# Performance work log

Measured on AMD Instinct MI355X. Metric: run time of the kernel, lower is better.

Reference implementation:

```python
import jax, jax.numpy as jnp
import numpy as np

E, C, K, S = 8, 128, 512, 512  # embedding_dim, channels, kernel_size, stride
NEG_SLOPE = 0.01  # torch F.leaky_relu default


def setup_inputs() -> dict:
    key = jax.random.key(0)
    ks = jax.random.split(key, 11)
    B, T = 4, 1_000_000
    sc = 0.05
    return {
        "x": jax.random.normal(ks[0], (B, T, E), jnp.float32),
        # ctx_conv: Conv1d(E, 2C, K, stride=S) -> weight (2C, E, K), bias (2C,)
        "ctx_conv_w": jax.random.normal(ks[1], (2 * C, E, K), jnp.float32) * sc,
        "ctx_conv_b": jax.random.normal(ks[2], (2 * C,), jnp.float32) * sc,
        # ctx_share: Conv1d(C, C, 1) -> (C, C) pointwise
        "ctx_share_w": jax.random.normal(ks[3], (C, C), jnp.float32) * sc,
        "ctx_share_b": jax.random.normal(ks[4], (C,), jnp.float32) * sc,
        "main_conv_w": jax.random.normal(ks[5], (2 * C, E, K), jnp.float32) * sc,
        "main_conv_b": jax.random.normal(ks[6], (2 * C,), jnp.float32) * sc,
        "main_share_w": jax.random.normal(ks[7], (C, C), jnp.float32) * sc,
        "main_share_b": jax.random.normal(ks[8], (C,), jnp.float32) * sc,
        # gct_proj: Linear(C, C) -> weight (C, C) (y = g @ W.T + b)
        "gct_proj_w": jax.random.normal(ks[9], (C, C), jnp.float32) * sc,
        "gct_proj_b": jax.random.normal(ks[10], (C,), jnp.float32) * sc,
    }


def _leaky(x):
    return jnp.where(x >= 0, x, NEG_SLOPE * x)


def _glu(x):  # GLU over channel dim 1
    a, b = jnp.split(x, 2, axis=1)
    return a * jax.nn.sigmoid(b)


def _conv(z, w, b):
    # z: (B, Cin, T), w: (Cout, Cin, K) -> (B, Cout, T_out), stride S, VALID
    y = jax.lax.conv_general_dilated(z, w, (S,), 'VALID',
                                     dimension_numbers=('NCH', 'OIH', 'NCH'))
    return y + b[None, :, None]


def _branch_act(z, wc, bc, ws, bs):
    # glu(conv(z)) -> leaky_relu(1x1 share conv)
    h = _glu(_conv(z, wc, bc))                                   # (B, C, T_out)
    h = _leaky(jnp.einsum('oc,bct->bot', ws, h) + bs[None, :, None])
    return h


def reference(x, ctx_conv_w, ctx_conv_b, ctx_share_w, ctx_share_b,
              main_conv_w, main_conv_b, main_share_w, main_share_b,
              gct_proj_w, gct_proj_b):
    z = jnp.transpose(x, (0, 2, 1))  # (B, E, T)
    # Context branch: global max over time of ctx activations (GCG context).
    g = _branch_act(z, ctx_conv_w, ctx_conv_b, ctx_share_w, ctx_share_b)
    gct = jnp.max(g, axis=-1)  # (B, C)
    # Main branch with global channel gating.
    h = _branch_act(z, main_conv_w, main_conv_b, main_share_w, main_share_b)  # (B, C, T_out)
    q = jnp.tanh(gct @ gct_proj_w.T + gct_proj_b)                # (B, C)
    gate = jax.nn.sigmoid(jnp.einsum('bct,bc->bt', h, q))        # (B, T_out)
    out = jnp.max(h * gate[:, None, :], axis=-1)                 # (B, C)
    return out
```

## Files before the change

### kernel.cpp

```cpp
#include <hip/hip_runtime.h>
#include <hip/hip_bf16.h>
#include <cmath>

#define B_    4
#define T_    1000000
#define E_    8
#define C_    128
#define NCH   512
#define KK    4096
#define TOUT  1953
#define TP    1956
#define TPAD  2048
#define NT2   31

typedef __attribute__((ext_vector_type(8))) short bf16x8;
typedef __attribute__((ext_vector_type(4))) float f32x4;

__device__ __forceinline__ float sigmoidf_(float v) { return 1.f / (1.f + __expf(-v)); }

__device__ __forceinline__ void gl2lds16(const void* g, void* l) {
  __builtin_amdgcn_global_load_lds((const __attribute__((address_space(1))) void*)g,
                                   (__attribute__((address_space(3))) void*)l, 16, 0, 0);
}

__global__ __launch_bounds__(256) void convert_x(const float* __restrict__ x,
                                                 __hip_bfloat16* __restrict__ xb) {
  size_t gid = (size_t)blockIdx.x * 256 + threadIdx.x;
  size_t idx8 = gid * 8;
  size_t b = idx8 >> 23;
  size_t rem = idx8 & ((1ull << 23) - 1);
  union { __hip_bfloat16 h[8]; uint4 u; } o;
  if (rem < (size_t)TOUT * KK) {
    const float* src = x + b * 8000000ull + rem;
    float4 f0 = *(const float4*)(src);
    float4 f1 = *(const float4*)(src + 4);
    o.h[0] = __float2bfloat16(f0.x); o.h[1] = __float2bfloat16(f0.y);
    o.h[2] = __float2bfloat16(f0.z); o.h[3] = __float2bfloat16(f0.w);
    o.h[4] = __float2bfloat16(f1.x); o.h[5] = __float2bfloat16(f1.y);
    o.h[6] = __float2bfloat16(f1.z); o.h[7] = __float2bfloat16(f1.w);
  } else {
    o.u = make_uint4(0, 0, 0, 0);
  }
  *(uint4*)(xb + idx8) = o.u;
}

__global__ __launch_bounds__(256) void prep_w(
    const float* __restrict__ wc, const float* __restrict__ bc,
    const float* __restrict__ wm, const float* __restrict__ bm,
    __hip_bfloat16* __restrict__ Wtb, float* __restrict__ bias_t) {
  __shared__ float row[KK];
  int n = blockIdx.x;
  int br = n >> 8, o = n & 255;
  const float* wsrc = (br ? wm : wc) + (size_t)o * KK;
  for (int i = threadIdx.x; i < KK; i += 256) row[i] = wsrc[i];
  __syncthreads();
  for (int i = threadIdx.x; i < KK; i += 256) {
    int kpos = i >> 3, e = i & 7;
    Wtb[(size_t)n * KK + i] = __float2bfloat16(row[e * 512 + kpos]);
  }
  if (threadIdx.x == 0) bias_t[n] = (br ? bm : bc)[o];
}

__global__ __launch_bounds__(256) void mfma_gemm(
    const __hip_bfloat16* __restrict__ xb, const __hip_bfloat16* __restrict__ Wtb,
    const float* __restrict__ bias_t, float* __restrict__ u2) {
  __shared__ __hip_bfloat16 As[128 * 32];
  __shared__ __hip_bfloat16 Bs[128 * 32];
  const int tid  = threadIdx.x;
  const int lane = tid & 63, wave = tid >> 6;
  const int wm = wave >> 1, wn = wave & 1;
  const int n0 = blockIdx.x * 128;
  const int t0 = blockIdx.y * 128;
  const int b  = blockIdx.z;

  const int r0 = tid >> 2;
  const int q8 = (tid & 3) * 8;
  const __hip_bfloat16* aS = xb + ((size_t)b * TPAD + (t0 + r0)) * KK + q8;
  const __hip_bfloat16* bS = Wtb + (size_t)(n0 + r0) * KK + q8;
  __hip_bfloat16* aD0 = As + (wave * 64) * 8;
  __hip_bfloat16* aD1 = As + (256 + wave * 64) * 8;
  __hip_bfloat16* bD0 = Bs + (wave * 64) * 8;
  __hip_bfloat16* bD1 = Bs + (256 + wave * 64) * 8;

  f32x4 acc[4][4];
#pragma unroll
  for (int i = 0; i < 4; ++i)
#pragma unroll
    for (int j = 0; j < 4; ++j) acc[i][j] = (f32x4)(0.0f);

  const int mrow = lane & 15;
  const int kq   = (lane >> 4) * 8;

  for (int k0 = 0; k0 < KK; k0 += 32) {
    __syncthreads();
    gl2lds16(aS + k0, aD0);
    gl2lds16(aS + 64 * KK + k0, aD1);
    gl2lds16(bS + k0, bD0);
    gl2lds16(bS + 64 * KK + k0, bD1);
    __syncthreads();

    bf16x8 af[4], bf[4];
#pragma unroll
    for (int i = 0; i < 4; ++i)
      af[i] = *(const bf16x8*)(As + (wm * 64 + i * 16 + mrow) * 32 + kq);
#pragma unroll
    for (int j = 0; j < 4; ++j)
      bf[j] = *(const bf16x8*)(Bs + (wn * 64 + j * 16 + mrow) * 32 + kq);
#pragma unroll
    for (int i = 0; i < 4; ++i)
#pragma unroll
      for (int j = 0; j < 4; ++j)
        acc[i][j] = __builtin_amdgcn_mfma_f32_16x16x32_bf16(af[i], bf[j], acc[i][j], 0, 0, 0);
  }

  const int crow = (lane >> 4) * 4;
  const int ccol = lane & 15;
#pragma unroll
  for (int j = 0; j < 4; ++j) {
    int n = n0 + wn * 64 + j * 16 + ccol;
    float bv = bias_t[n];
    float* urow = u2 + ((size_t)n * 4 + b) * TP;
#pragma unroll
    for (int i = 0; i < 4; ++i) {
      int bt = t0 + wm * 64 + i * 16 + crow;
      if (bt < TOUT) {
        f32x4 v = acc[i][j];
        v.x += bv; v.y += bv; v.z += bv; v.w += bv;
        *(f32x4*)(urow + bt) = v;
      }
    }
  }
}

__global__ __launch_bounds__(256) void share_act(
    const float* __restrict__ u2,
    const float* __restrict__ wsc, const float* __restrict__ bsc,
    const float* __restrict__ wsm, const float* __restrict__ bsm,
    float* __restrict__ hmain, float* __restrict__ gct_part) {
  __shared__ float Wl[128 * 132];
  __shared__ float ul[128 * 68];
  const int tid  = threadIdx.x;
  const int tile = blockIdx.x;
  const int b    = blockIdx.y;
  const int br   = blockIdx.z;
  const int t0   = tile * 64;
  const float* ws = br ? wsm : wsc;
  const float* bs = br ? bsm : bsc;

  for (int g = tid; g < 16384; g += 256) {
    int co = g >> 7, cp = g & 127;
    Wl[cp * 132 + co] = ws[g];
  }
  const size_t base_v = ((size_t)(br * 256) * 4 + b) * TP;
  const size_t base_g = ((size_t)(br * 256 + 128) * 4 + b) * TP;
  for (int g = tid; g < 8192; g += 256) {
    int cp = g >> 6, t = g & 63;
    float v = 0.f;
    if (t0 + t < TOUT) {
      float va = u2[base_v + (size_t)cp * 4 * TP + t0 + t];
      float vg = u2[base_g + (size_t)cp * 4 * TP + t0 + t];
      v = va * sigmoidf_(vg);
    }
    ul[cp * 68 + t] = v;
  }
  __syncthreads();

  const int ty = tid >> 4, tx = tid & 15;
  float acc[8][4];
#pragma unroll
  for (int i = 0; i < 8; ++i)
#pragma unroll
    for (int j = 0; j < 4; ++j) acc[i][j] = 0.f;

  for (int cp = 0; cp < 128; ++cp) {
    float4 a0 = *(const float4*)&Wl[cp*132 + ty*4];
    float4 a1 = *(const float4*)&Wl[cp*132 + 64 + ty*4];
    float4 b4 = *(const float4*)&ul[cp*68 + tx*4];
    float av[8] = {a0.x,a0.y,a0.z,a0.w,a1.x,a1.y,a1.z,a1.w};
    float bv[4] = {b4.x,b4.y,b4.z,b4.w};
#pragma unroll
    for (int i = 0; i < 8; ++i)
#pragma unroll
      for (int j = 0; j < 4; ++j) acc[i][j] = fmaf(av[i], bv[j], acc[i][j]);
  }

  float mloc[8];
#pragma unroll
  for (int i = 0; i < 8; ++i) mloc[i] = -INFINITY;
#pragma unroll
  for (int i = 0; i < 8; ++i) {
    int c = (i < 4) ? (ty*4 + i) : (64 + ty*4 + (i - 4));
    float bias = bs[c];
#pragma unroll
    for (int j = 0; j < 4; ++j) {
      int t = t0 + tx*4 + j;
      if (t >= TOUT) continue;
      float v = acc[i][j] + bias;
      v = (v >= 0.f) ? v : 0.01f * v;
      if (br == 1) {
        hmain[((size_t)b * 128 + c) * TOUT + t] = v;
      } else {
        mloc[i] = fmaxf(mloc[i], v);
      }
    }
  }
  if (br == 0) {
    __syncthreads();
    float* red = ul;
#pragma unroll
    for (int i = 0; i < 8; ++i) {
      int c = (i < 4) ? (ty*4 + i) : (64 + ty*4 + (i - 4));
      red[c * 16 + tx] = mloc[i];
    }
    __syncthreads();
    if (tid < 128) {
      float m = -INFINITY;
#pragma unroll
      for (int k = 0; k < 16; ++k) m = fmaxf(m, red[tid * 16 + k]);
      gct_part[((size_t)b * 128 + tid) * NT2 + tile] = m;
    }
  }
}

__global__ void gct_q(const float* __restrict__ gct_part, const float* __restrict__ wp,
                      const float* __restrict__ bp, float* __restrict__ q) {
  int b = blockIdx.x, tid = threadIdx.x;
  __shared__ float g[128];
  float m = -INFINITY;
  for (int tl = 0; tl < NT2; ++tl) m = fmaxf(m, gct_part[((size_t)b * 128 + tid) * NT2 + tl]);
  g[tid] = m;
  __syncthreads();
  float s = bp[tid];
  for (int c = 0; c < 128; ++c) s = fmaf(g[c], wp[tid * 128 + c], s);
  q[b * 128 + tid] = tanhf(s);
}

__global__ __launch_bounds__(256) void gate_max(
    const float* __restrict__ hmain, const float* __restrict__ q,
    float* __restrict__ out_part) {
  __shared__ float hl[128 * 68];
  __shared__ float ql[128];
  __shared__ float red[256];
  __shared__ float gl[64];
  int tid = threadIdx.x, tile = blockIdx.x, b = blockIdx.y;
  int t0 = tile * 64;
  for (int g = tid; g < 8192; g += 256) {
    int c = g >> 6, t = g & 63;
    hl[c * 68 + t] = (t0 + t < TOUT) ? hmain[((size_t)b * 128 + c) * TOUT + t0 + t] : 0.f;
  }
  if (tid < 128) ql[tid] = q[b * 128 + tid];
  __syncthreads();
  {
    int t = tid & 63, cy = tid >> 6;
    float s = 0.f;
#pragma unroll
    for (int cc = 0; cc < 32; ++cc) s = fmaf(hl[(cy * 32 + cc) * 68 + t], ql[cy * 32 + cc], s);
    red[cy * 64 + t] = s;
  }
  __syncthreads();
  if (tid < 64) {
    float s = red[tid] + red[64 + tid] + red[128 + tid] + red[192 + tid];
    gl[tid] = sigmoidf_(s);
  }
  __syncthreads();
  {
    int c = tid >> 1, th = tid & 1;
    float m = -INFINITY;
#pragma unroll
    for (int tt = 0; tt < 32; ++tt) {
      int t = th * 32 + tt;
      if (t0 + t < TOUT) m = fmaxf(m, hl[c * 68 + t] * gl[t]);
    }
    red[c * 2 + th] = m;
  }
  __syncthreads();
  if (tid < 128) out_part[((size_t)b * 128 + tid) * NT2 + tile] = fmaxf(red[tid * 2], red[tid * 2 + 1]);
}

__global__ void final_max(const float* __restrict__ out_part, float* __restrict__ out) {
  int idx = blockIdx.x * 256 + threadIdx.x;
  if (idx < 512) {
    float m = -INFINITY;
    for (int tl = 0; tl < NT2; ++tl) m = fmaxf(m, out_part[(size_t)idx * NT2 + tl]);
    out[idx] = m;
  }
}

extern "C" void kernel_launch(void* const* d_in, const int* in_sizes, int n_in,
                              void* d_out, int out_size, void* d_ws, size_t ws_size,
                              hipStream_t stream) {
  const float* x      = (const float*)d_in[0];
  const float* ctx_w  = (const float*)d_in[1];
  const float* ctx_b  = (const float*)d_in[2];
  const float* ctx_sw = (const float*)d_in[3];
  const float* ctx_sb = (const float*)d_in[4];
  const float* main_w = (const float*)d_in[5];
  const float* main_b = (const float*)d_in[6];
  const float* main_sw= (const float*)d_in[7];
  const float* main_sb= (const float*)d_in[8];
  const float* gp_w   = (const float*)d_in[9];
  const float* gp_b   = (const float*)d_in[10];

  char* w = (char*)d_ws;
  __hip_bfloat16* xb  = (__hip_bfloat16*)(w);
  __hip_bfloat16* Wtb = (__hip_bfloat16*)(w + 67108864);
  float* bias_t  = (float*)(w + 71303168);
  float* u2      = (float*)(w + 71305216);
  float* hmain   = (float*)(w + 87328768);
  float* gct_part= (float*)(w + 91328512);
  float* q       = (float*)(w + 91392000);
  float* out_part= (float*)(w + 91394048);

  convert_x<<<16384, 256, 0, stream>>>(x, xb);
  prep_w<<<NCH, 256, 0, stream>>>(ctx_w, ctx_b, main_w, main_b, Wtb, bias_t);
  mfma_gemm<<<dim3(4, 16, B_), 256, 0, stream>>>(xb, Wtb, bias_t, u2);
  share_act<<<dim3(NT2, B_, 2), 256, 0, stream>>>(u2, ctx_sw, ctx_sb, main_sw, main_sb,
                                                  hmain, gct_part);
  gct_q<<<B_, 128, 0, stream>>>(gct_part, gp_w, gp_b, q);
  gate_max<<<dim3(NT2, B_), 256, 0, stream>>>(hmain, q, out_part);
  final_max<<<2, 256, 0, stream>>>(out_part, (float*)d_out);
}
```

Baseline: 354.3 us.

## Fuse x bf16 conversion into GEMM, split-K by two, double-buffer LDS

```diff
diff --git a/kernel.cpp b/kernel.cpp
--- a/kernel.cpp
+++ b/kernel.cpp
@@ -8,10 +8,11 @@
 #define C_    128
 #define NCH   512
 #define KK    4096
+#define KH    2048
 #define TOUT  1953
 #define TP    1956
-#define TPAD  2048
 #define NT2   31
+#define KSOFF ((size_t)NCH * B_ * TP)
 
 typedef __attribute__((ext_vector_type(8))) short bf16x8;
 typedef __attribute__((ext_vector_type(4))) float f32x4;
@@ -21,27 +22,6 @@
 __device__ __forceinline__ void gl2lds16(const void* g, void* l) {
   __builtin_amdgcn_global_load_lds((const __attribute__((address_space(1))) void*)g,
                                    (__attribute__((address_space(3))) void*)l, 16, 0, 0);
-}
-
-__global__ __launch_bounds__(256) void convert_x(const float* __restrict__ x,
-                                                 __hip_bfloat16* __restrict__ xb) {
-  size_t gid = (size_t)blockIdx.x * 256 + threadIdx.x;
-  size_t idx8 = gid * 8;
-  size_t b = idx8 >> 23;
-  size_t rem = idx8 & ((1ull << 23) - 1);
-  union { __hip_bfloat16 h[8]; uint4 u; } o;
-  if (rem < (size_t)TOUT * KK) {
-    const float* src = x + b * 8000000ull + rem;
-    float4 f0 = *(const float4*)(src);
-    float4 f1 = *(const float4*)(src + 4);
-    o.h[0] = __float2bfloat16(f0.x); o.h[1] = __float2bfloat16(f0.y);
-    o.h[2] = __float2bfloat16(f0.z); o.h[3] = __float2bfloat16(f0.w);
-    o.h[4] = __float2bfloat16(f1.x); o.h[5] = __float2bfloat16(f1.y);
-    o.h[6] = __float2bfloat16(f1.z); o.h[7] = __float2bfloat16(f1.w);
-  } else {
-    o.u = make_uint4(0, 0, 0, 0);
-  }
-  *(uint4*)(xb + idx8) = o.u;
 }
 
 __global__ __launch_bounds__(256) void prep_w(
@@ -61,26 +41,30 @@
   if (threadIdx.x == 0) bias_t[n] = (br ? bm : bc)[o];
 }
 
-__global__ __launch_bounds__(256) void mfma_gemm(
-    const __hip_bfloat16* __restrict__ xb, const __hip_bfloat16* __restrict__ Wtb,
-    const float* __restrict__ bias_t, float* __restrict__ u2) {
-  __shared__ __hip_bfloat16 As[128 * 32];
-  __shared__ __hip_bfloat16 Bs[128 * 32];
+__global__ __launch_bounds__(256, 2) void mfma_gemm(
+    const float* __restrict__ x, const __hip_bfloat16* __restrict__ Wtb,
+    float* __restrict__ u2) {
+  __shared__ __hip_bfloat16 As[2][128 * 32];
+  __shared__ __hip_bfloat16 Bs[2][128 * 32];
   const int tid  = threadIdx.x;
   const int lane = tid & 63, wave = tid >> 6;
   const int wm = wave >> 1, wn = wave & 1;
   const int n0 = blockIdx.x * 128;
   const int t0 = blockIdx.y * 128;
-  const int b  = blockIdx.z;
+  const int bz = blockIdx.z;
+  const int b  = bz >> 1, ks = bz & 1;
+  const size_t kbase = (size_t)ks * KH;
 
   const int r0 = tid >> 2;
   const int q8 = (tid & 3) * 8;
-  const __hip_bfloat16* aS = xb + ((size_t)b * TPAD + (t0 + r0)) * KK + q8;
-  const __hip_bfloat16* bS = Wtb + (size_t)(n0 + r0) * KK + q8;
-  __hip_bfloat16* aD0 = As + (wave * 64) * 8;
-  __hip_bfloat16* aD1 = As + (256 + wave * 64) * 8;
-  __hip_bfloat16* bD0 = Bs + (wave * 64) * 8;
-  __hip_bfloat16* bD1 = Bs + (256 + wave * 64) * 8;
+  const __hip_bfloat16* bS = Wtb + (size_t)(n0 + r0) * KK + kbase + q8;
+
+  const int ar = tid >> 2;
+  const int ac = (tid & 3) * 8;
+  int row0 = t0 + ar;      if (row0 > TOUT - 1) row0 = TOUT - 1;
+  int row1 = t0 + 64 + ar; if (row1 > TOUT - 1) row1 = TOUT - 1;
+  const float* aP0 = x + (size_t)b * 8000000ull + (size_t)row0 * KK + kbase + ac;
+  const float* aP1 = x + (size_t)b * 8000000ull + (size_t)row1 * KK + kbase + ac;
 
   f32x4 acc[4][4];
 #pragma unroll
@@ -91,26 +75,63 @@
   const int mrow = lane & 15;
   const int kq   = (lane >> 4) * 8;
 
-  for (int k0 = 0; k0 < KK; k0 += 32) {
+  float4 a0, a1, a2, a3;
+  a0 = *(const float4*)(aP0);     a1 = *(const float4*)(aP0 + 4);
+  a2 = *(const float4*)(aP1);     a3 = *(const float4*)(aP1 + 4);
+  gl2lds16(bS,           &Bs[0][wave * 512]);
+  gl2lds16(bS + 64 * KK, &Bs[0][2048 + wave * 512]);
+  {
+    union { __hip_bfloat16 h[8]; bf16x8 v; } u0, u1;
+    u0.h[0]=__float2bfloat16(a0.x); u0.h[1]=__float2bfloat16(a0.y);
+    u0.h[2]=__float2bfloat16(a0.z); u0.h[3]=__float2bfloat16(a0.w);
+    u0.h[4]=__float2bfloat16(a1.x); u0.h[5]=__float2bfloat16(a1.y);
+    u0.h[6]=__float2bfloat16(a1.z); u0.h[7]=__float2bfloat16(a1.w);
+    u1.h[0]=__float2bfloat16(a2.x); u1.h[1]=__float2bfloat16(a2.y);
+    u1.h[2]=__float2bfloat16(a2.z); u1.h[3]=__float2bfloat16(a2.w);
+    u1.h[4]=__float2bfloat16(a3.x); u1.h[5]=__float2bfloat16(a3.y);
+    u1.h[6]=__float2bfloat16(a3.z); u1.h[7]=__float2bfloat16(a3.w);
+    *(bf16x8*)&As[0][tid * 8]        = u0.v;
+    *(bf16x8*)&As[0][2048 + tid * 8] = u1.v;
+  }
+
+  for (int s = 0; s < KH / 32; ++s) {
+    const int cur = s & 1, nxt = cur ^ 1;
     __syncthreads();
-    gl2lds16(aS + k0, aD0);
-    gl2lds16(aS + 64 * KK + k0, aD1);
-    gl2lds16(bS + k0, bD0);
-    gl2lds16(bS + 64 * KK + k0, bD1);
-    __syncthreads();
+    if (s < KH / 32 - 1) {
+      gl2lds16(bS + (s + 1) * 32,           &Bs[nxt][wave * 512]);
+      gl2lds16(bS + (s + 1) * 32 + 64 * KK, &Bs[nxt][2048 + wave * 512]);
+      a0 = *(const float4*)(aP0 + (s + 1) * 32);
+      a1 = *(const float4*)(aP0 + (s + 1) * 32 + 4);
+      a2 = *(const float4*)(aP1 + (s + 1) * 32);
+      a3 = *(const float4*)(aP1 + (s + 1) * 32 + 4);
+    }
 
     bf16x8 af[4], bf[4];
 #pragma unroll
     for (int i = 0; i < 4; ++i)
-      af[i] = *(const bf16x8*)(As + (wm * 64 + i * 16 + mrow) * 32 + kq);
+      af[i] = *(const bf16x8*)&As[cur][(wm * 64 + i * 16 + mrow) * 32 + kq];
 #pragma unroll
     for (int j = 0; j < 4; ++j)
-      bf[j] = *(const bf16x8*)(Bs + (wn * 64 + j * 16 + mrow) * 32 + kq);
+      bf[j] = *(const bf16x8*)&Bs[cur][(wn * 64 + j * 16 + mrow) * 32 + kq];
 #pragma unroll
     for (int i = 0; i < 4; ++i)
 #pragma unroll
       for (int j = 0; j < 4; ++j)
         acc[i][j] = __builtin_amdgcn_mfma_f32_16x16x32_bf16(af[i], bf[j], acc[i][j], 0, 0, 0);
+
+    if (s < KH / 32 - 1) {
+      union { __hip_bfloat16 h[8]; bf16x8 v; } u0, u1;
+      u0.h[0]=__float2bfloat16(a0.x); u0.h[1]=__float2bfloat16(a0.y);
+      u0.h[2]=__float2bfloat16(a0.z); u0.h[3]=__float2bfloat16(a0.w);
+      u0.h[4]=__float2bfloat16(a1.x); u0.h[5]=__float2bfloat16(a1.y);
+      u0.h[6]=__float2bfloat16(a1.z); u0.h[7]=__float2bfloat16(a1.w);
+      u1.h[0]=__float2bfloat16(a2.x); u1.h[1]=__float2bfloat16(a2.y);
+      u1.h[2]=__float2bfloat16(a2.z); u1.h[3]=__float2bfloat16(a2.w);
+      u1.h[4]=__float2bfloat16(a3.x); u1.h[5]=__float2bfloat16(a3.y);
+      u1.h[6]=__float2bfloat16(a3.z); u1.h[7]=__float2bfloat16(a3.w);
+      *(bf16x8*)&As[nxt][tid * 8]        = u0.v;
+      *(bf16x8*)&As[nxt][2048 + tid * 8] = u1.v;
+    }
   }
 
   const int crow = (lane >> 4) * 4;
@@ -118,22 +139,17 @@
 #pragma unroll
   for (int j = 0; j < 4; ++j) {
     int n = n0 + wn * 64 + j * 16 + ccol;
-    float bv = bias_t[n];
-    float* urow = u2 + ((size_t)n * 4 + b) * TP;
+    float* urow = u2 + ((size_t)(ks * NCH + n) * B_ + b) * TP;
 #pragma unroll
     for (int i = 0; i < 4; ++i) {
       int bt = t0 + wm * 64 + i * 16 + crow;
-      if (bt < TOUT) {
-        f32x4 v = acc[i][j];
-        v.x += bv; v.y += bv; v.z += bv; v.w += bv;
-        *(f32x4*)(urow + bt) = v;
-      }
+      if (bt < TOUT) *(f32x4*)(urow + bt) = acc[i][j];
     }
   }
 }
 
 __global__ __launch_bounds__(256) void share_act(
-    const float* __restrict__ u2,
+    const float* __restrict__ u2, const float* __restrict__ bias_t,
     const float* __restrict__ wsc, const float* __restrict__ bsc,
     const float* __restrict__ wsm, const float* __restrict__ bsm,
     float* __restrict__ hmain, float* __restrict__ gct_part) {
@@ -151,14 +167,16 @@
     int co = g >> 7, cp = g & 127;
     Wl[cp * 132 + co] = ws[g];
   }
-  const size_t base_v = ((size_t)(br * 256) * 4 + b) * TP;
-  const size_t base_g = ((size_t)(br * 256 + 128) * 4 + b) * TP;
+  const size_t base_v = ((size_t)(br * 256) * B_ + b) * TP;
+  const size_t base_g = ((size_t)(br * 256 + 128) * B_ + b) * TP;
   for (int g = tid; g < 8192; g += 256) {
     int cp = g >> 6, t = g & 63;
     float v = 0.f;
     if (t0 + t < TOUT) {
-      float va = u2[base_v + (size_t)cp * 4 * TP + t0 + t];
-      float vg = u2[base_g + (size_t)cp * 4 * TP + t0 + t];
+      size_t ov = base_v + (size_t)cp * B_ * TP + t0 + t;
+      size_t og = base_g + (size_t)cp * B_ * TP + t0 + t;
+      float va = u2[ov] + u2[KSOFF + ov] + bias_t[br * 256 + cp];
+      float vg = u2[og] + u2[KSOFF + og] + bias_t[br * 256 + 128 + cp];
       v = va * sigmoidf_(vg);
     }
     ul[cp * 68 + t] = v;
@@ -302,20 +320,18 @@
   const float* gp_b   = (const float*)d_in[10];
 
   char* w = (char*)d_ws;
-  __hip_bfloat16* xb  = (__hip_bfloat16*)(w);
-  __hip_bfloat16* Wtb = (__hip_bfloat16*)(w + 67108864);
-  float* bias_t  = (float*)(w + 71303168);
-  float* u2      = (float*)(w + 71305216);
-  float* hmain   = (float*)(w + 87328768);
-  float* gct_part= (float*)(w + 91328512);
-  float* q       = (float*)(w + 91392000);
-  float* out_part= (float*)(w + 91394048);
-
-  convert_x<<<16384, 256, 0, stream>>>(x, xb);
+  __hip_bfloat16* Wtb = (__hip_bfloat16*)(w);
+  float* bias_t  = (float*)(w + 4194304);
+  float* u2      = (float*)(w + 4196352);
+  float* hmain   = (float*)(w + 36243456);
+  float* gct_part= (float*)(w + 40243200);
+  float* q       = (float*)(w + 40306688);
+  float* out_part= (float*)(w + 40308736);
+
   prep_w<<<NCH, 256, 0, stream>>>(ctx_w, ctx_b, main_w, main_b, Wtb, bias_t);
-  mfma_gemm<<<dim3(4, 16, B_), 256, 0, stream>>>(xb, Wtb, bias_t, u2);
-  share_act<<<dim3(NT2, B_, 2), 256, 0, stream>>>(u2, ctx_sw, ctx_sb, main_sw, main_sb,
-                                                  hmain, gct_part);
+  mfma_gemm<<<dim3(4, 16, B_ * 2), 256, 0, stream>>>(x, Wtb, u2);
+  share_act<<<dim3(NT2, B_, 2), 256, 0, stream>>>(u2, bias_t, ctx_sw, ctx_sb,
+                                                  main_sw, main_sb, hmain, gct_part);
   gct_q<<<B_, 128, 0, stream>>>(gct_part, gp_w, gp_b, q);
   gate_max<<<dim3(NT2, B_), 256, 0, stream>>>(hmain, q, out_part);
   final_max<<<2, 256, 0, stream>>>(out_part, (float*)d_out);
```

New measurement: 354.9 us. No clear change (+0.2%).

## Pre-swizzle operands into MFMA fragment layout and load directly to registers

Applied to the files above, without the earlier changes.

```diff
diff --git a/kernel.cpp b/kernel.cpp
--- a/kernel.cpp
+++ b/kernel.cpp
@@ -18,99 +18,111 @@
 
 __device__ __forceinline__ float sigmoidf_(float v) { return 1.f / (1.f + __expf(-v)); }
 
-__device__ __forceinline__ void gl2lds16(const void* g, void* l) {
-  __builtin_amdgcn_global_load_lds((const __attribute__((address_space(1))) void*)g,
-                                   (__attribute__((address_space(3))) void*)l, 16, 0, 0);
-}
-
-__global__ __launch_bounds__(256) void convert_x(const float* __restrict__ x,
-                                                 __hip_bfloat16* __restrict__ xb) {
-  size_t gid = (size_t)blockIdx.x * 256 + threadIdx.x;
-  size_t idx8 = gid * 8;
-  size_t b = idx8 >> 23;
-  size_t rem = idx8 & ((1ull << 23) - 1);
-  union { __hip_bfloat16 h[8]; uint4 u; } o;
-  if (rem < (size_t)TOUT * KK) {
-    const float* src = x + b * 8000000ull + rem;
-    float4 f0 = *(const float4*)(src);
-    float4 f1 = *(const float4*)(src + 4);
-    o.h[0] = __float2bfloat16(f0.x); o.h[1] = __float2bfloat16(f0.y);
-    o.h[2] = __float2bfloat16(f0.z); o.h[3] = __float2bfloat16(f0.w);
-    o.h[4] = __float2bfloat16(f1.x); o.h[5] = __float2bfloat16(f1.y);
-    o.h[6] = __float2bfloat16(f1.z); o.h[7] = __float2bfloat16(f1.w);
-  } else {
-    o.u = make_uint4(0, 0, 0, 0);
-  }
-  *(uint4*)(xb + idx8) = o.u;
-}
-
-__global__ __launch_bounds__(256) void prep_w(
+__global__ __launch_bounds__(256) void prep_inputs(
+    const float* __restrict__ x,
     const float* __restrict__ wc, const float* __restrict__ bc,
     const float* __restrict__ wm, const float* __restrict__ bm,
-    __hip_bfloat16* __restrict__ Wtb, float* __restrict__ bias_t) {
+    __hip_bfloat16* __restrict__ xb2, __hip_bfloat16* __restrict__ Wn2,
+    float* __restrict__ bias_t) {
   __shared__ float row[KK];
-  int n = blockIdx.x;
-  int br = n >> 8, o = n & 255;
-  const float* wsrc = (br ? wm : wc) + (size_t)o * KK;
-  for (int i = threadIdx.x; i < KK; i += 256) row[i] = wsrc[i];
-  __syncthreads();
-  for (int i = threadIdx.x; i < KK; i += 256) {
-    int kpos = i >> 3, e = i & 7;
-    Wtb[(size_t)n * KK + i] = __float2bfloat16(row[e * 512 + kpos]);
-  }
-  if (threadIdx.x == 0) bias_t[n] = (br ? bm : bc)[o];
-}
-
-__global__ __launch_bounds__(256) void mfma_gemm(
-    const __hip_bfloat16* __restrict__ xb, const __hip_bfloat16* __restrict__ Wtb,
-    const float* __restrict__ bias_t, float* __restrict__ u2) {
-  __shared__ __hip_bfloat16 As[128 * 32];
-  __shared__ __hip_bfloat16 Bs[128 * 32];
+  const int bid = blockIdx.x;
+  if (bid < NCH) {
+    const int n = bid, br = n >> 8, o = n & 255;
+    const float* wsrc = (br ? wm : wc) + (size_t)o * KK;
+    for (int i = threadIdx.x; i < KK; i += 256) row[i] = wsrc[i];
+    __syncthreads();
+    const int nt = n >> 4, nr = n & 15;
+    for (int k = threadIdx.x; k < KK; k += 256) {
+      int kpos = k >> 3, e = k & 7;
+      size_t addr = (((size_t)nt * 128 + (k >> 5)) * 64
+                     + (size_t)((k >> 3) & 3) * 16 + nr) * 8 + (k & 7);
+      Wn2[addr] = __float2bfloat16(row[e * 512 + kpos]);
+    }
+    if (threadIdx.x == 0) bias_t[n] = (br ? bm : bc)[o];
+  } else {
+    size_t gid = (size_t)(bid - NCH) * 256 + threadIdx.x;
+    size_t idx8 = gid * 8;
+    size_t b = idx8 >> 23, rem = idx8 & ((1ull << 23) - 1);
+    int lane = (int)((rem >> 3) & 63);
+    int kc   = (int)((rem >> 9) & 127);
+    int tt   = (int)(rem >> 16);
+    int t = tt * 16 + (lane & 15);
+    int k = kc * 32 + (lane >> 4) * 8;
+    union { __hip_bfloat16 h[8]; uint4 u; } o;
+    if (t < TOUT) {
+      const float* src = x + b * 8000000ull + (size_t)t * KK + k;
+      float4 f0 = *(const float4*)(src);
+      float4 f1 = *(const float4*)(src + 4);
+      o.h[0] = __float2bfloat16(f0.x); o.h[1] = __float2bfloat16(f0.y);
+      o.h[2] = __float2bfloat16(f0.z); o.h[3] = __float2bfloat16(f0.w);
+      o.h[4] = __float2bfloat16(f1.x); o.h[5] = __float2bfloat16(f1.y);
+      o.h[6] = __float2bfloat16(f1.z); o.h[7] = __float2bfloat16(f1.w);
+    } else {
+      o.u = make_uint4(0, 0, 0, 0);
+    }
+    *(uint4*)(xb2 + idx8) = o.u;
+  }
+}
+
+__global__ __launch_bounds__(512, 2) void mfma_gemm(
+    const __hip_bfloat16* __restrict__ xb2, const __hip_bfloat16* __restrict__ Wn2,
+    float* __restrict__ u2) {
   const int tid  = threadIdx.x;
   const int lane = tid & 63, wave = tid >> 6;
-  const int wm = wave >> 1, wn = wave & 1;
-  const int n0 = blockIdx.x * 128;
-  const int t0 = blockIdx.y * 128;
-  const int b  = blockIdx.z;
-
-  const int r0 = tid >> 2;
-  const int q8 = (tid & 3) * 8;
-  const __hip_bfloat16* aS = xb + ((size_t)b * TPAD + (t0 + r0)) * KK + q8;
-  const __hip_bfloat16* bS = Wtb + (size_t)(n0 + r0) * KK + q8;
-  __hip_bfloat16* aD0 = As + (wave * 64) * 8;
-  __hip_bfloat16* aD1 = As + (256 + wave * 64) * 8;
-  __hip_bfloat16* bD0 = Bs + (wave * 64) * 8;
-  __hip_bfloat16* bD1 = Bs + (256 + wave * 64) * 8;
-
-  f32x4 acc[4][4];
-#pragma unroll
-  for (int i = 0; i < 4; ++i)
+  const int wt = wave & 3, wn = wave >> 2;
+
+  const int L   = blockIdx.x;
+  const int xcd = L & 7;
+  const int r   = L >> 3;
+  const int nb  = r & 3;
+  const int sh  = r >> 2;
+  const int s   = sh * 8 + xcd;
+  const int tblk = s & 15, b = s >> 4;
+  const int t0 = tblk * 128, n0 = nb * 128;
+
+  const size_t FR = 512;
+  const __hip_bfloat16* aB = xb2
+      + ((size_t)(b * 128 + (t0 >> 4) + wt * 2) * 128) * FR + (size_t)lane * 8;
+  const __hip_bfloat16* bB = Wn2
+      + ((size_t)((n0 >> 4) + wn * 4) * 128) * FR + (size_t)lane * 8;
+
+  f32x4 acc[2][4];
+#pragma unroll
+  for (int i = 0; i < 2; ++i)
 #pragma unroll
     for (int j = 0; j < 4; ++j) acc[i][j] = (f32x4)(0.0f);
 
-  const int mrow = lane & 15;
-  const int kq   = (lane >> 4) * 8;
-
-  for (int k0 = 0; k0 < KK; k0 += 32) {
-    __syncthreads();
-    gl2lds16(aS + k0, aD0);
-    gl2lds16(aS + 64 * KK + k0, aD1);
-    gl2lds16(bS + k0, bD0);
-    gl2lds16(bS + 64 * KK + k0, bD1);
-    __syncthreads();
-
-    bf16x8 af[4], bf[4];
-#pragma unroll
-    for (int i = 0; i < 4; ++i)
-      af[i] = *(const bf16x8*)(As + (wm * 64 + i * 16 + mrow) * 32 + kq);
+  bf16x8 A0[2][2], B0[4][2], A1[2][2], B1[4][2];
+
+  auto load_set = [&](bf16x8 (&aF)[2][2], bf16x8 (&bF)[4][2], int kc) {
+#pragma unroll
+    for (int i = 0; i < 2; ++i)
+#pragma unroll
+      for (int c = 0; c < 2; ++c)
+        aF[i][c] = *(const bf16x8*)(aB + (size_t)(i * 128 + kc + c) * FR);
 #pragma unroll
     for (int j = 0; j < 4; ++j)
-      bf[j] = *(const bf16x8*)(Bs + (wn * 64 + j * 16 + mrow) * 32 + kq);
-#pragma unroll
-    for (int i = 0; i < 4; ++i)
-#pragma unroll
-      for (int j = 0; j < 4; ++j)
-        acc[i][j] = __builtin_amdgcn_mfma_f32_16x16x32_bf16(af[i], bf[j], acc[i][j], 0, 0, 0);
+#pragma unroll
+      for (int c = 0; c < 2; ++c)
+        bF[j][c] = *(const bf16x8*)(bB + (size_t)(j * 128 + kc + c) * FR);
+  };
+  auto do_mfma = [&](bf16x8 (&aF)[2][2], bf16x8 (&bF)[4][2]) {
+#pragma unroll
+    for (int c = 0; c < 2; ++c)
+#pragma unroll
+      for (int i = 0; i < 2; ++i)
+#pragma unroll
+        for (int j = 0; j < 4; ++j)
+          acc[i][j] = __builtin_amdgcn_mfma_f32_16x16x32_bf16(aF[i][c], bF[j][c],
+                                                              acc[i][j], 0, 0, 0);
+  };
+
+  load_set(A0, B0, 0);
+  for (int kc = 0; kc < 128; kc += 4) {
+    load_set(A1, B1, kc + 2);
+    do_mfma(A0, B0);
+    if (kc + 4 < 128) load_set(A0, B0, kc + 4);
+    do_mfma(A1, B1);
   }
 
   const int crow = (lane >> 4) * 4;
@@ -118,22 +130,17 @@
 #pragma unroll
   for (int j = 0; j < 4; ++j) {
     int n = n0 + wn * 64 + j * 16 + ccol;
-    float bv = bias_t[n];
-    float* urow = u2 + ((size_t)n * 4 + b) * TP;
-#pragma unroll
-    for (int i = 0; i < 4; ++i) {
-      int bt = t0 + wm * 64 + i * 16 + crow;
-      if (bt < TOUT) {
-        f32x4 v = acc[i][j];
-        v.x += bv; v.y += bv; v.z += bv; v.w += bv;
-        *(f32x4*)(urow + bt) = v;
-      }
+    float* urow = u2 + ((size_t)n * B_ + b) * TP;
+#pragma unroll
+    for (int i = 0; i < 2; ++i) {
+      int t = t0 + wt * 32 + i * 16 + crow;
+      if (t < TOUT) *(f32x4*)(urow + t) = acc[i][j];
     }
   }
 }
 
 __global__ __launch_bounds__(256) void share_act(
-    const float* __restrict__ u2,
+    const float* __restrict__ u2, const float* __restrict__ bias_t,
     const float* __restrict__ wsc, const float* __restrict__ bsc,
     const float* __restrict__ wsm, const float* __restrict__ bsm,
     float* __restrict__ hmain, float* __restrict__ gct_part) {
@@ -151,14 +158,14 @@
     int co = g >> 7, cp = g & 127;
     Wl[cp * 132 + co] = ws[g];
   }
-  const size_t base_v = ((size_t)(br * 256) * 4 + b) * TP;
-  const size_t base_g = ((size_t)(br * 256 + 128) * 4 + b) * TP;
+  const size_t base_v = ((size_t)(br * 256) * B_ + b) * TP;
+  const size_t base_g = ((size_t)(br * 256 + 128) * B_ + b) * TP;
   for (int g = tid; g < 8192; g += 256) {
     int cp = g >> 6, t = g & 63;
     float v = 0.f;
     if (t0 + t < TOUT) {
-      float va = u2[base_v + (size_t)cp * 4 * TP + t0 + t];
-      float vg = u2[base_g + (size_t)cp * 4 * TP + t0 + t];
+      float va = u2[base_v + (size_t)cp * B_ * TP + t0 + t] + bias_t[br * 256 + cp];
+      float vg = u2[base_g + (size_t)cp * B_ * TP + t0 + t] + bias_t[br * 256 + 128 + cp];
       v = va * sigmoidf_(vg);
     }
     ul[cp * 68 + t] = v;
@@ -302,8 +309,8 @@
   const float* gp_b   = (const float*)d_in[10];
 
   char* w = (char*)d_ws;
-  __hip_bfloat16* xb  = (__hip_bfloat16*)(w);
-  __hip_bfloat16* Wtb = (__hip_bfloat16*)(w + 67108864);
+  __hip_bfloat16* xb2 = (__hip_bfloat16*)(w);
+  __hip_bfloat16* Wn2 = (__hip_bfloat16*)(w + 67108864);
   float* bias_t  = (float*)(w + 71303168);
   float* u2      = (float*)(w + 71305216);
   float* hmain   = (float*)(w + 87328768);
@@ -311,11 +318,11 @@
   float* q       = (float*)(w + 91392000);
   float* out_part= (float*)(w + 91394048);
 
-  convert_x<<<16384, 256, 0, stream>>>(x, xb);
-  prep_w<<<NCH, 256, 0, stream>>>(ctx_w, ctx_b, main_w, main_b, Wtb, bias_t);
-  mfma_gemm<<<dim3(4, 16, B_), 256, 0, stream>>>(xb, Wtb, bias_t, u2);
-  share_act<<<dim3(NT2, B_, 2), 256, 0, stream>>>(u2, ctx_sw, ctx_sb, main_sw, main_sb,
-                                                  hmain, gct_part);
+  prep_inputs<<<NCH + 16384, 256, 0, stream>>>(x, ctx_w, ctx_b, main_w, main_b,
+                                               xb2, Wn2, bias_t);
+  mfma_gemm<<<256, 512, 0, stream>>>(xb2, Wn2, u2);
+  share_act<<<dim3(NT2, B_, 2), 256, 0, stream>>>(u2, bias_t, ctx_sw, ctx_sb,
+                                                  main_sw, main_sb, hmain, gct_part);
   gct_q<<<B_, 128, 0, stream>>>(gct_part, gp_w, gp_b, q);
   gate_max<<<dim3(NT2, B_), 256, 0, stream>>>(hmain, q, out_part);
   final_max<<<2, 256, 0, stream>>>(out_part, (float*)d_out);
```

After: 315.8 us. 1.12x faster.
